# Kernel optimization log

Measured on AMD Instinct MI355X. Metric: run time of the kernel, lower is better.

The kernel has to match this reference:

```python
import jax, jax.numpy as jnp
import numpy as np

N_NODES = 50000
N_EDGES = 800000
F_IN = 32
H = 128
N_REL = 4
MAX_DEG = 10
N_GRAPHS = 64
N_BLOCKS = 2


def setup_inputs() -> dict:
    key = jax.random.key(0)
    ks = jax.random.split(key, 20)
    s = 0.05
    return {
        "x": jax.random.normal(ks[0], (N_NODES, F_IN), jnp.float32),
        "edge_index": jax.random.randint(ks[1], (2, N_EDGES), 0, N_NODES, dtype=jnp.int32),
        "edge_attr": jax.random.randint(ks[2], (N_EDGES,), 0, N_REL, dtype=jnp.int32),
        "batch_idx": jnp.sort(jax.random.randint(ks[3], (N_NODES,), 0, N_GRAPHS, dtype=jnp.int32)),
        "embed_W": jax.random.normal(ks[4], (F_IN, H), jnp.float32) * s,
        "embed_b": jax.random.normal(ks[5], (H,), jnp.float32) * s,
        "rgcn_Wrel": jax.random.normal(ks[6], (N_BLOCKS, N_REL, H, H), jnp.float32) * s,
        "rgcn_Wroot": jax.random.normal(ks[7], (N_BLOCKS, H, H), jnp.float32) * s,
        "rgcn_b": jax.random.normal(ks[8], (N_BLOCKS, H), jnp.float32) * s,
        "mf_Wl": jax.random.normal(ks[9], (N_BLOCKS, MAX_DEG + 1, H, H), jnp.float32) * s,
        "mf_bl": jax.random.normal(ks[10], (N_BLOCKS, MAX_DEG + 1, H), jnp.float32) * s,
        "mf_Wr": jax.random.normal(ks[11], (N_BLOCKS, MAX_DEG + 1, H, H), jnp.float32) * s,
        "lin1_W": jax.random.normal(ks[12], (H, H), jnp.float32) * s,
        "lin1_b": jax.random.normal(ks[13], (H,), jnp.float32) * s,
        "lin2_W": jax.random.normal(ks[14], (H, 1), jnp.float32) * s,
        "lin2_b": jax.random.normal(ks[15], (1,), jnp.float32) * s,
    }


def _rgcn(x, src, dst, rel, Wrel, Wroot, b):
    # PyG RGCNConv with default aggr='mean': per-relation mean over incoming
    # edges, then per-relation weight, plus root transform and bias.
    seg = dst * N_REL + rel  # composite segment id: (node, relation)
    agg = jax.ops.segment_sum(x[src], seg, num_segments=N_NODES * N_REL)
    cnt = jax.ops.segment_sum(jnp.ones((seg.shape[0],), x.dtype), seg,
                              num_segments=N_NODES * N_REL)
    agg = (agg / jnp.maximum(cnt, 1.0)[:, None]).reshape(N_NODES, N_REL, H)
    return jnp.einsum('nrh,rho->no', agg, Wrel) + x @ Wroot + b


def _mfconv(x, src, dst, Wl, bl, Wr):
    # PyG MFConv: sum-aggregate neighbors, then per-degree-bucket linear heads
    # (degree = in-degree clamped to MAX_DEG); lin_r applied to root x (no bias).
    h = jax.ops.segment_sum(x[src], dst, num_segments=N_NODES)  # [N,H]
    deg = jax.ops.segment_sum(jnp.ones((src.shape[0],), jnp.int32), dst,
                              num_segments=N_NODES)
    deg = jnp.minimum(deg, MAX_DEG)  # [N]
    # out_all: [D+1, N, H] candidate outputs, one per degree bucket
    out_all = (jnp.einsum('nh,dho->dno', h, Wl)
               + jnp.einsum('nh,dho->dno', x, Wr)
               + bl[:, None, :])
    return jnp.take_along_axis(out_all, deg[None, :, None], axis=0)[0]


def reference(x, edge_index, edge_attr, batch_idx, embed_W, embed_b,
              rgcn_Wrel, rgcn_Wroot, rgcn_b, mf_Wl, mf_bl, mf_Wr,
              lin1_W, lin1_b, lin2_W, lin2_b):
    src, dst = edge_index[0], edge_index[1]
    h = x @ embed_W + embed_b
    for blk in range(N_BLOCKS):
        if blk > 0:  # first block uses Identity instead of ReLU
            h = jax.nn.relu(h)
        h = _rgcn(h, src, dst, edge_attr, rgcn_Wrel[blk], rgcn_Wroot[blk], rgcn_b[blk])
        h = jax.nn.relu(h)
        h = _mfconv(h, src, dst, mf_Wl[blk], mf_bl[blk], mf_Wr[blk])
    g = jax.ops.segment_sum(h, batch_idx, num_segments=N_GRAPHS)  # global_add_pool
    g = jax.nn.relu(g @ lin1_W + lin1_b)
    return g @ lin2_W + lin2_b
```

## Files before the change

kernel.cpp:

```cpp
#include <hip/hip_runtime.h>
#include <hip/hip_bf16.h>

#define NRELS 4
#define MAXDEG 10
#define NBUCK 11
#define POOL_CHUNKS 8

typedef __attribute__((ext_vector_type(8))) short s16x8;
typedef __attribute__((ext_vector_type(4))) float f32x4;
typedef __attribute__((ext_vector_type(8))) unsigned short u16x8;

__device__ inline unsigned short f2b(float f) {
  __hip_bfloat16 h = __float2bfloat16(f);
  return *reinterpret_cast<unsigned short*>(&h);
}
__device__ inline float b2f(unsigned short u) {
  union { unsigned int i; float f; } v;
  v.i = ((unsigned int)u) << 16;
  return v.f;
}
__device__ inline float blo(unsigned int v) {
  union { unsigned int i; float f; } x;
  x.i = v << 16;
  return x.f;
}
__device__ inline float bhi(unsigned int v) {
  union { unsigned int i; float f; } x;
  x.i = v & 0xffff0000u;
  return x.f;
}

typedef __attribute__((address_space(3))) unsigned int lds_uint;
typedef __attribute__((address_space(1))) const unsigned int glob_uint;
__device__ __forceinline__ void gld_lds16(const void* g, void* l) {
  __builtin_amdgcn_global_load_lds((glob_uint*)g, (lds_uint*)l, 16, 0, 0);
}

__global__ __launch_bounds__(512) void coarse_count_scan(
    const int* __restrict__ dst, int* __restrict__ bhist, int* __restrict__ boff,
    int* __restrict__ bcur, int* __restrict__ done, int* __restrict__ perm, int permCap,
    int NB, int E, int nblocks) {
  __shared__ int lh[512];
  __shared__ int lastf;
  int t = threadIdx.x;
  lh[t] = 0;
  __syncthreads();
  for (int i = blockIdx.x * 512 + t; i < permCap; i += nblocks * 512) perm[i] = -1;
  int base = blockIdx.x * 4096;
  int lim = E - base;
  if (lim > 4096) lim = 4096;
  for (int i = t; i < lim; i += 512) atomicAdd(&lh[dst[base + i] >> 7], 1);
  __syncthreads();
  if (lh[t]) atomicAdd(&bhist[t], lh[t]);
  __threadfence();
  __syncthreads();
  if (t == 0) lastf = (atomicAdd(done, 1) == nblocks - 1) ? 1 : 0;
  __syncthreads();
  if (!lastf) return;
  int v = (t < NB) ? atomicAdd(&bhist[t], 0) : 0;
  lh[t] = v;
  __syncthreads();
  for (int o = 1; o < 512; o <<= 1) {
    int x = (t >= o) ? lh[t - o] : 0;
    __syncthreads();
    lh[t] += x;
    __syncthreads();
  }
  if (t < NB) {
    int st = lh[t] - v;
    boff[t] = st;
    bcur[t] = st;
  }
  if (t == 0) boff[NB] = E;
}

__global__ __launch_bounds__(512) void coarse_scatter(
    const int* __restrict__ src, const int* __restrict__ dst, const int* __restrict__ rel,
    int* __restrict__ bcur, uint2* __restrict__ ebuf, int E) {
  __shared__ int lhist[512];
  __shared__ int lstart[512];
  __shared__ int lcur[512];
  __shared__ int gbase[512];
  __shared__ uint2 stage[4096];
  int t = threadIdx.x;
  lhist[t] = 0;
  __syncthreads();
  int base = blockIdx.x * 4096;
  int lim = E - base;
  if (lim > 4096) lim = 4096;
  for (int i = t; i < lim; i += 512) atomicAdd(&lhist[dst[base + i] >> 7], 1);
  __syncthreads();
  int myc = lhist[t];
  lstart[t] = myc;
  __syncthreads();
  for (int o = 1; o < 512; o <<= 1) {
    int x = (t >= o) ? lstart[t - o] : 0;
    __syncthreads();
    lstart[t] += x;
    __syncthreads();
  }
  int incl = lstart[t];
  __syncthreads();
  lstart[t] = incl - myc;
  lcur[t] = 0;
  if (myc > 0) gbase[t] = atomicAdd(&bcur[t], myc);
  __syncthreads();
  for (int i = t; i < lim; i += 512) {
    int e = base + i;
    int d = dst[e];
    int b = d >> 7;
    int slot = lstart[b] + atomicAdd(&lcur[b], 1);
    stage[slot] = make_uint2((unsigned)(d * 4 + rel[e]), (unsigned)src[e]);
  }
  __syncthreads();
  for (int i = t; i < lim; i += 512) {
    uint2 val = stage[i];
    int b = (int)(val.x >> 9);
    ebuf[gbase[b] + (i - lstart[b])] = val;
  }
}

__global__ __launch_bounds__(512) void fine_place(
    const uint2* __restrict__ ebuf, const int* __restrict__ boff, int* __restrict__ cnt,
    int* __restrict__ seg_start, float* __restrict__ inv, int* __restrict__ deg,
    int* __restrict__ bucket, int* __restrict__ hist, int* __restrict__ csr, int NSEG) {
  __shared__ int lh[512];
  __shared__ int sc[512];
  __shared__ int lcur[512];
  __shared__ int lbh[16];
  int t = threadIdx.x;
  int b = blockIdx.x;
  lh[t] = 0;
  if (t < 16) lbh[t] = 0;
  __syncthreads();
  int s = boff[b], e = boff[b + 1];
  for (int i = s + t; i < e; i += 512) atomicAdd(&lh[ebuf[i].x & 511], 1);
  __syncthreads();
  int v = lh[t];
  sc[t] = v;
  __syncthreads();
  for (int o = 1; o < 512; o <<= 1) {
    int x = (t >= o) ? sc[t - o] : 0;
    __syncthreads();
    sc[t] += x;
    __syncthreads();
  }
  int gseg = b * 512 + t;
  int mystart = s + sc[t] - v;
  lcur[t] = mystart;
  if (gseg < NSEG) {
    cnt[gseg] = v;
    seg_start[gseg] = mystart;
    inv[gseg] = 1.0f / (float)(v > 1 ? v : 1);
    if ((t & 3) == 0) {
      int d = sc[t + 3] - sc[t] + v;
      int n = gseg >> 2;
      deg[n] = d;
      int bk = d < MAXDEG ? d : MAXDEG;
      bucket[n] = bk;
      atomicAdd(&lbh[bk], 1);
    }
  }
  __syncthreads();
  if (t < NBUCK && lbh[t]) atomicAdd(&hist[t], lbh[t]);
  for (int i = s + t; i < e; i += 512) {
    uint2 vv = ebuf[i];
    int pos = atomicAdd(&lcur[vv.x & 511], 1);
    csr[pos] = (int)vv.y;
  }
}

__global__ void build_perm(const int* __restrict__ bucket, const int* __restrict__ hist,
                           int* __restrict__ fill, int* __restrict__ perm, int N) {
  __shared__ int soff[NBUCK];
  if (threadIdx.x == 0) {
    int acc = 0;
    for (int b = 0; b < NBUCK; b++) {
      soff[b] = acc;
      acc += ((hist[b] + 63) >> 6) << 6;
    }
  }
  __syncthreads();
  int n = blockIdx.x * 256 + threadIdx.x;
  int b = (n < N) ? bucket[n] : -1;
  int lane = threadIdx.x & 63;
  for (int bb = 0; bb < NBUCK; bb++) {
    unsigned long long m = __ballot(b == bb);
    if (m == 0ULL) continue;
    int leader = __ffsll(m) - 1;
    int base = 0;
    if (lane == leader) base = atomicAdd(&fill[bb], __popcll(m));
    base = __shfl(base, leader);
    if (b == bb) {
      int idx = __popcll(m & ((1ULL << lane) - 1ULL));
      perm[soff[bb] + base + idx] = n;
    }
  }
}

__global__ __launch_bounds__(256) void embed_conv(
    const float* __restrict__ x, const float* __restrict__ embW,
    const float* __restrict__ bias, const float* __restrict__ Wrel,
    const float* __restrict__ Wroot, const float* __restrict__ Wl,
    const float* __restrict__ Wr, unsigned short* __restrict__ Bt,
    unsigned short* __restrict__ Btm, unsigned short* __restrict__ out, int N, int nbE) {
  if ((int)blockIdx.x >= nbE) {
    const int R1 = 2 * 128 * 640;
    const int R2 = R1 + 2 * 11 * 128 * 256;
    int t = (blockIdx.x - nbE) * 256 + threadIdx.x;
    if (t < R1) {
      int blk = t / 81920;
      int rem = t % 81920;
      int n = rem / 640;
      int k = rem % 640;
      float v;
      if (k < 512)
        v = Wrel[(size_t)blk * 65536 + (size_t)k * 128 + n];
      else
        v = Wroot[(size_t)blk * 16384 + (size_t)(k - 512) * 128 + n];
      Bt[t] = f2b(v);
    } else if (t < R2) {
      int t2 = t - R1;
      int k = t2 & 255;
      int n = (t2 >> 8) & 127;
      int bb = (t2 >> 15) % 11;
      int blk = t2 / (11 * 128 * 256);
      float v;
      if (k < 128)
        v = Wl[(((size_t)blk * 11 + bb) * 128 + k) * 128 + n];
      else
        v = Wr[(((size_t)blk * 11 + bb) * 128 + (k - 128)) * 128 + n];
      Btm[t2] = f2b(v);
    }
    return;
  }
  __shared__ unsigned char As[64 * 80];
  __shared__ unsigned char Bs[128 * 80];
  int t = threadIdx.x;
  int m0 = blockIdx.x * 64;
  {
    int r = t >> 2, s = t & 3;
    int gr = m0 + r;
    if (gr >= N) gr = N - 1;
    const float* xp = x + (size_t)gr * 32 + s * 8;
    float4 f0 = *(const float4*)xp;
    float4 f1 = *(const float4*)(xp + 4);
    u16x8 o;
    o[0] = f2b(f0.x); o[1] = f2b(f0.y); o[2] = f2b(f0.z); o[3] = f2b(f0.w);
    o[4] = f2b(f1.x); o[5] = f2b(f1.y); o[6] = f2b(f1.z); o[7] = f2b(f1.w);
    *(u16x8*)(As + r * 80 + s * 16) = o;
  }
  {
    int n = t >> 1, hf = t & 1;
    unsigned short tmp[16];
#pragma unroll
    for (int j = 0; j < 16; j++) tmp[j] = f2b(embW[(size_t)(hf * 16 + j) * 128 + n]);
    *(u16x8*)(Bs + n * 80 + hf * 32) = *(u16x8*)tmp;
    *(u16x8*)(Bs + n * 80 + hf * 32 + 16) = *(u16x8*)(tmp + 8);
  }
  __syncthreads();
  int lane = t & 63, wave = t >> 6;
  int row = lane & 15, quad = lane >> 4;
  int nh = wave * 32;
  f32x4 acc[2][4];
#pragma unroll
  for (int i = 0; i < 2; i++)
#pragma unroll
    for (int j = 0; j < 4; j++) acc[i][j] = (f32x4){0.f, 0.f, 0.f, 0.f};
  s16x8 af[4], bf[2];
#pragma unroll
  for (int mt = 0; mt < 4; mt++) {
    int R = mt * 16 + row;
    af[mt] = *(const s16x8*)(As + R * 80 + quad * 16);
  }
#pragma unroll
  for (int nt = 0; nt < 2; nt++) {
    int R = nh + nt * 16 + row;
    bf[nt] = *(const s16x8*)(Bs + R * 80 + quad * 16);
  }
#pragma unroll
  for (int nt = 0; nt < 2; nt++)
#pragma unroll
    for (int mt = 0; mt < 4; mt++)
      acc[nt][mt] = __builtin_amdgcn_mfma_f32_16x16x32_bf16(af[mt], bf[nt], acc[nt][mt], 0, 0, 0);
#pragma unroll
  for (int nt = 0; nt < 2; nt++) {
    int n = nh + nt * 16 + row;
    float bv = bias[n];
#pragma unroll
    for (int mt = 0; mt < 4; mt++) {
#pragma unroll
      for (int r4 = 0; r4 < 4; r4++) {
        int m = m0 + mt * 16 + quad * 4 + r4;
        if (m < N) out[(size_t)m * 128 + n] = f2b(acc[nt][mt][r4] + bv);
      }
    }
  }
}

#define ACC8(v)                                   \
  do {                                            \
    a0 += blo((v).x); a1 += bhi((v).x);           \
    a2 += blo((v).y); a3 += bhi((v).y);           \
    a4 += blo((v).z); a5 += bhi((v).z);           \
    a6 += blo((v).w); a7 += bhi((v).w);           \
  } while (0)

__global__ __launch_bounds__(256) void rgcn_gather(
    const unsigned short* __restrict__ hb, const int* __restrict__ csr,
    const int* __restrict__ seg_start, const int* __restrict__ cnt,
    const float* __restrict__ inv, const int* __restrict__ perm,
    unsigned short* __restrict__ ahat, int total) {
  int half = blockIdx.x & 1;
  int i = (blockIdx.x >> 1) * 32 + (threadIdx.x >> 3);
  if (i >= total) return;
  int n = perm[i];
  if (n < 0) return;
  int c8 = half * 64 + (threadIdx.x & 7) * 8;
  int4 st4 = *(const int4*)(seg_start + (size_t)n * 4);
  int4 cn4 = *(const int4*)(cnt + (size_t)n * 4);
  float4 w4 = *(const float4*)(inv + (size_t)n * 4);
  int sts[4] = {st4.x, st4.y, st4.z, st4.w};
  int cns[4] = {cn4.x, cn4.y, cn4.z, cn4.w};
  float ws[4] = {w4.x, w4.y, w4.z, w4.w};
#pragma unroll
  for (int r = 0; r < 4; r++) {
    int st = sts[r], cn = cns[r];
    float w = ws[r];
    float a0 = 0.f, a1 = 0.f, a2 = 0.f, a3 = 0.f, a4 = 0.f, a5 = 0.f, a6 = 0.f, a7 = 0.f;
    int ii = 0;
    for (; ii + 4 <= cn; ii += 4) {
      int p0 = csr[st + ii], p1 = csr[st + ii + 1];
      int p2 = csr[st + ii + 2], p3 = csr[st + ii + 3];
      uint4 v0 = *(const uint4*)(hb + (size_t)p0 * 128 + c8);
      uint4 v1 = *(const uint4*)(hb + (size_t)p1 * 128 + c8);
      uint4 v2 = *(const uint4*)(hb + (size_t)p2 * 128 + c8);
      uint4 v3 = *(const uint4*)(hb + (size_t)p3 * 128 + c8);
      ACC8(v0);
      ACC8(v1);
      ACC8(v2);
      ACC8(v3);
    }
    if (ii + 2 <= cn) {
      int p0 = csr[st + ii], p1 = csr[st + ii + 1];
      uint4 v0 = *(const uint4*)(hb + (size_t)p0 * 128 + c8);
      uint4 v1 = *(const uint4*)(hb + (size_t)p1 * 128 + c8);
      ACC8(v0);
      ACC8(v1);
      ii += 2;
    }
    if (ii < cn) {
      uint4 v0 = *(const uint4*)(hb + (size_t)csr[st + ii] * 128 + c8);
      ACC8(v0);
    }
    uint4 o;
    o.x = (unsigned int)f2b(a0 * w) | ((unsigned int)f2b(a1 * w) << 16);
    o.y = (unsigned int)f2b(a2 * w) | ((unsigned int)f2b(a3 * w) << 16);
    o.z = (unsigned int)f2b(a4 * w) | ((unsigned int)f2b(a5 * w) << 16);
    o.w = (unsigned int)f2b(a6 * w) | ((unsigned int)f2b(a7 * w) << 16);
    *(uint4*)(ahat + (size_t)i * 512 + r * 128 + c8) = o;
  }
}

__global__ __launch_bounds__(256) void mf_gather(
    const unsigned short* __restrict__ hb, const int* __restrict__ csr,
    const int* __restrict__ seg_start, const int* __restrict__ deg,
    const int* __restrict__ perm, unsigned short* __restrict__ amf, int total) {
  int half = blockIdx.x & 1;
  int i = (blockIdx.x >> 1) * 32 + (threadIdx.x >> 3);
  if (i >= total) return;
  int n = perm[i];
  if (n < 0) return;
  int c8 = half * 64 + (threadIdx.x & 7) * 8;
  int st = seg_start[n * 4], dg = deg[n];
  float a0 = 0.f, a1 = 0.f, a2 = 0.f, a3 = 0.f, a4 = 0.f, a5 = 0.f, a6 = 0.f, a7 = 0.f;
  int i2 = 0;
  for (; i2 + 4 <= dg; i2 += 4) {
    int p0 = csr[st + i2], p1 = csr[st + i2 + 1];
    int p2 = csr[st + i2 + 2], p3 = csr[st + i2 + 3];
    uint4 v0 = *(const uint4*)(hb + (size_t)p0 * 128 + c8);
    uint4 v1 = *(const uint4*)(hb + (size_t)p1 * 128 + c8);
    uint4 v2 = *(const uint4*)(hb + (size_t)p2 * 128 + c8);
    uint4 v3 = *(const uint4*)(hb + (size_t)p3 * 128 + c8);
    ACC8(v0);
    ACC8(v1);
    ACC8(v2);
    ACC8(v3);
  }
  if (i2 + 2 <= dg) {
    int p0 = csr[st + i2], p1 = csr[st + i2 + 1];
    uint4 v0 = *(const uint4*)(hb + (size_t)p0 * 128 + c8);
    uint4 v1 = *(const uint4*)(hb + (size_t)p1 * 128 + c8);
    ACC8(v0);
    ACC8(v1);
    i2 += 2;
  }
  if (i2 < dg) {
    uint4 v0 = *(const uint4*)(hb + (size_t)csr[st + i2] * 128 + c8);
    ACC8(v0);
  }
  uint4 o;
  o.x = (unsigned int)f2b(a0) | ((unsigned int)f2b(a1) << 16);
  o.y = (unsigned int)f2b(a2) | ((unsigned int)f2b(a3) << 16);
  o.z = (unsigned int)f2b(a4) | ((unsigned int)f2b(a5) << 16);
  o.w = (unsigned int)f2b(a6) | ((unsigned int)f2b(a7) << 16);
  *(uint4*)(amf + (size_t)i * 128 + c8) = o;
}

__global__ __launch_bounds__(256) void rgcn_mfma(const unsigned short* __restrict__ A,
                                                 const unsigned short* __restrict__ hroot,
                                                 const unsigned short* __restrict__ Bt,
                                                 const float* __restrict__ bias,
                                                 const int* __restrict__ perm,
                                                 unsigned short* __restrict__ out) {
  __shared__ unsigned char As[8192];
  __shared__ unsigned char Bs[16384];
  __shared__ int nodes[64];
  int t = threadIdx.x;
  int m0 = blockIdx.x * 64;
  if (t >= 64 && t < 128) nodes[t - 64] = perm[m0 + t - 64];
  __syncthreads();
  int lane = t & 63, wave = t >> 6;
  int row = lane & 15, quad = lane >> 4;
  int nh = wave * 32;
  f32x4 acc[2][4];
#pragma unroll
  for (int i = 0; i < 2; i++)
#pragma unroll
    for (int j = 0; j < 4; j++) acc[i][j] = (f32x4){0.f, 0.f, 0.f, 0.f};

  for (int kt = 0; kt < 10; kt++) {
    int kb2 = kt * 128;
#pragma unroll
    for (int s = 0; s < 2; s++) {
      int o = s * 4096 + t * 16;
      int r = o >> 7, c = ((o >> 4) & 7) ^ (r & 7);
      const char* gsrc;
      if (kt < 8) {
        gsrc = (const char*)A + (size_t)(m0 + r) * 1024 + kb2 + c * 16;
      } else {
        int nd = nodes[r];
        if (nd < 0) nd = 0;
        gsrc = (const char*)hroot + (size_t)nd * 256 + (kb2 - 1024) + c * 16;
      }
      gld_lds16(gsrc, As + o);
    }
#pragma unroll
    for (int s = 0; s < 4; s++) {
      int o = s * 4096 + t * 16;
      int r = o >> 7, c = ((o >> 4) & 7) ^ (r & 7);
      gld_lds16((const char*)Bt + (size_t)r * 1280 + kb2 + c * 16, Bs + o);
    }
    __syncthreads();
#pragma unroll
    for (int ks = 0; ks < 2; ks++) {
      int cch = ks * 4 + quad;
      s16x8 af[4], bf[2];
#pragma unroll
      for (int mt = 0; mt < 4; mt++) {
        int R = mt * 16 + row;
        af[mt] = *(const s16x8*)(As + R * 128 + ((cch ^ (R & 7)) << 4));
      }
#pragma unroll
      for (int nt = 0; nt < 2; nt++) {
        int R = nh + nt * 16 + row;
        bf[nt] = *(const s16x8*)(Bs + R * 128 + ((cch ^ (R & 7)) << 4));
      }
#pragma unroll
      for (int nt = 0; nt < 2; nt++)
#pragma unroll
        for (int mt = 0; mt < 4; mt++)
          acc[nt][mt] = __builtin_amdgcn_mfma_f32_16x16x32_bf16(af[mt], bf[nt], acc[nt][mt], 0, 0, 0);
    }
    __syncthreads();
  }
#pragma unroll
  for (int nt = 0; nt < 2; nt++) {
    int n = nh + nt * 16 + row;
    float bv = bias[n];
#pragma unroll
    for (int mt = 0; mt < 4; mt++) {
#pragma unroll
      for (int r4 = 0; r4 < 4; r4++) {
        int nd = nodes[mt * 16 + quad * 4 + r4];
        if (nd >= 0) out[(size_t)nd * 128 + n] = f2b(fmaxf(acc[nt][mt][r4] + bv, 0.f));
      }
    }
  }
}

__global__ __launch_bounds__(256) void mf_mfma(const unsigned short* __restrict__ A,
                                               const unsigned short* __restrict__ hroot,
                                               const unsigned short* __restrict__ Bt,
                                               const float* __restrict__ bl,
                                               const int* __restrict__ perm,
                                               const int* __restrict__ hist,
                                               unsigned short* __restrict__ out, int relu_out) {
  __shared__ unsigned char As[8192];
  __shared__ unsigned char Bs[16384];
  __shared__ int soff[NBUCK + 1];
  __shared__ int nodes[64];
  int t = threadIdx.x;
  int m0 = blockIdx.x * 64;
  if (t == 0) {
    int acc = 0;
    for (int b2 = 0; b2 < NBUCK; b2++) {
      soff[b2] = acc;
      acc += ((hist[b2] + 63) >> 6) << 6;
    }
    soff[NBUCK] = acc;
  }
  if (t >= 64 && t < 128) nodes[t - 64] = perm[m0 + t - 64];
  __syncthreads();
  if (m0 >= soff[NBUCK]) return;
  int b = 0;
  while (b < 10 && m0 >= soff[b + 1]) b++;
  const unsigned short* Bb = Bt + (size_t)b * 128 * 256;
  const float* bb = bl + b * 128;
  int lane = t & 63, wave = t >> 6;
  int row = lane & 15, quad = lane >> 4;
  int nh = wave * 32;
  f32x4 acc[2][4];
#pragma unroll
  for (int i = 0; i < 2; i++)
#pragma unroll
    for (int j = 0; j < 4; j++) acc[i][j] = (f32x4){0.f, 0.f, 0.f, 0.f};

  for (int kt = 0; kt < 4; kt++) {
    int kb2 = kt * 128;
#pragma unroll
    for (int s = 0; s < 2; s++) {
      int o = s * 4096 + t * 16;
      int r = o >> 7, c = ((o >> 4) & 7) ^ (r & 7);
      const char* gsrc;
      if (kt < 2) {
        gsrc = (const char*)A + (size_t)(m0 + r) * 256 + kb2 + c * 16;
      } else {
        int nd = nodes[r];
        if (nd < 0) nd = 0;
        gsrc = (const char*)hroot + (size_t)nd * 256 + (kb2 - 512) + c * 16;
      }
      gld_lds16(gsrc, As + o);
    }
#pragma unroll
    for (int s = 0; s < 4; s++) {
      int o = s * 4096 + t * 16;
      int r = o >> 7, c = ((o >> 4) & 7) ^ (r & 7);
      gld_lds16((const char*)Bb + (size_t)r * 512 + kb2 + c * 16, Bs + o);
    }
    __syncthreads();
#pragma unroll
    for (int ks = 0; ks < 2; ks++) {
      int cch = ks * 4 + quad;
      s16x8 af[4], bf[2];
#pragma unroll
      for (int mt = 0; mt < 4; mt++) {
        int R = mt * 16 + row;
        af[mt] = *(const s16x8*)(As + R * 128 + ((cch ^ (R & 7)) << 4));
      }
#pragma unroll
      for (int nt = 0; nt < 2; nt++) {
        int R = nh + nt * 16 + row;
        bf[nt] = *(const s16x8*)(Bs + R * 128 + ((cch ^ (R & 7)) << 4));
      }
#pragma unroll
      for (int nt = 0; nt < 2; nt++)
#pragma unroll
        for (int mt = 0; mt < 4; mt++)
          acc[nt][mt] = __builtin_amdgcn_mfma_f32_16x16x32_bf16(af[mt], bf[nt], acc[nt][mt], 0, 0, 0);
    }
    __syncthreads();
  }
#pragma unroll
  for (int nt = 0; nt < 2; nt++) {
    int n = nh + nt * 16 + row;
    float bv = bb[n];
#pragma unroll
    for (int mt = 0; mt < 4; mt++) {
#pragma unroll
      for (int r4 = 0; r4 < 4; r4++) {
        int nd = nodes[mt * 16 + quad * 4 + r4];
        if (nd >= 0) {
          float v = acc[nt][mt][r4] + bv;
          if (relu_out) v = fmaxf(v, 0.f);
          out[(size_t)nd * 128 + n] = f2b(v);
        }
      }
    }
  }
}

__global__ void pool2(const unsigned short* __restrict__ h, const int* __restrict__ batch,
                      float* __restrict__ g, int N, int G) {
  int gr = blockIdx.x / POOL_CHUNKS;
  int ck = blockIdx.x % POOL_CHUNKS;
  int t = threadIdx.x;
  int lane = t & 63, grp = t >> 6;
  int lo = 0, hi = N;
  while (lo < hi) {
    int m = (lo + hi) >> 1;
    if (batch[m] < gr) lo = m + 1; else hi = m;
  }
  int s = lo;
  lo = s; hi = N;
  while (lo < hi) {
    int m = (lo + hi) >> 1;
    if (batch[m] < gr + 1) lo = m + 1; else hi = m;
  }
  int e = lo;
  int len = e - s;
  int a = s + (int)(((long long)len * ck) / POOL_CHUNKS);
  int b = s + (int)(((long long)len * (ck + 1)) / POOL_CHUNKS);
  float s0 = 0.f, s1 = 0.f;
  for (int n = a + grp; n < b; n += 2) {
    unsigned int v = *(const unsigned int*)(h + (size_t)n * 128 + lane * 2);
    s0 += blo(v);
    s1 += bhi(v);
  }
  if (b > a + grp) {
    atomicAdd(&g[gr * 128 + lane * 2], s0);
    atomicAdd(&g[gr * 128 + lane * 2 + 1], s1);
  }
}

__global__ void head_kernel(const float* __restrict__ g, const float* __restrict__ W1,
                            const float* __restrict__ b1, const float* __restrict__ W2,
                            const float* __restrict__ b2, float* __restrict__ out) {
  int bg = blockIdx.x;
  int o = threadIdx.x;
  __shared__ float gs[128];
  __shared__ float red[128];
  gs[o] = g[bg * 128 + o];
  __syncthreads();
  float acc = b1[o];
  for (int k = 0; k < 128; k++) acc += gs[k] * W1[k * 128 + o];
  acc = fmaxf(acc, 0.f);
  red[o] = acc * W2[o];
  __syncthreads();
  for (int s = 64; s > 0; s >>= 1) {
    if (o < s) red[o] += red[o + s];
    __syncthreads();
  }
  if (o == 0) out[bg] = red[0] + b2[0];
}

extern "C" void kernel_launch(void* const* d_in, const int* in_sizes, int n_in,
                              void* d_out, int out_size, void* d_ws, size_t ws_size,
                              hipStream_t stream) {
  const float* x = (const float*)d_in[0];
  const int* ei = (const int*)d_in[1];
  const int* ea = (const int*)d_in[2];
  const int* batch = (const int*)d_in[3];
  const float* embW = (const float*)d_in[4];
  const float* embB = (const float*)d_in[5];
  const float* Wrel = (const float*)d_in[6];
  const float* Wroot = (const float*)d_in[7];
  const float* rb = (const float*)d_in[8];
  const float* Wl = (const float*)d_in[9];
  const float* bl = (const float*)d_in[10];
  const float* Wr = (const float*)d_in[11];
  const float* l1W = (const float*)d_in[12];
  const float* l1b = (const float*)d_in[13];
  const float* l2W = (const float*)d_in[14];
  const float* l2b = (const float*)d_in[15];
  float* out = (float*)d_out;

  int N = in_sizes[0] / 32;
  int E = in_sizes[2];
  int G = out_size;
  int NSEG = N * 4;
  int NB = (N + 127) >> 7;

  char* p = (char*)d_ws;
  auto alloc = [&](size_t bytes) {
    char* r = p;
    p += (bytes + 255) & ~(size_t)255;
    return r;
  };
  int permCap = ((N + 63) / 64 + NBUCK) * 64;
  unsigned short* h_bf = (unsigned short*)alloc((size_t)N * 128 * 2);
  unsigned short* h2_bf = (unsigned short*)alloc((size_t)N * 128 * 2);
  unsigned short* ahat = (unsigned short*)alloc((size_t)permCap * 512 * 2);
  unsigned short* amf = (unsigned short*)alloc((size_t)permCap * 128 * 2);
  unsigned short* Btr = (unsigned short*)alloc((size_t)2 * 128 * 640 * 2);
  unsigned short* Btm = (unsigned short*)alloc((size_t)2 * 11 * 128 * 256 * 2);
  float* inv = (float*)alloc((size_t)NSEG * 4);
  int* cnt = (int*)alloc((size_t)NSEG * 4);
  int* seg_start = (int*)alloc((size_t)NSEG * 4);
  int* csr = (int*)alloc((size_t)E * 4);
  uint2* ebuf = (uint2*)alloc((size_t)E * 8);
  int* deg = (int*)alloc((size_t)N * 4);
  int* bucket = (int*)alloc((size_t)N * 4);
  int* perm = (int*)alloc((size_t)permCap * 4);
  int* boff = (int*)alloc(516 * 4);
  int* bcur = (int*)alloc(512 * 4);
  size_t zeroBytes = 8192 + (size_t)G * 128 * 4;
  char* zb = alloc(zeroBytes);
  int* bhist = (int*)zb;
  int* hist = (int*)(zb + 4096);
  int* fill = (int*)(zb + 4224);
  int* done = (int*)(zb + 4352);
  float* g = (float*)(zb + 8192);

  (void)hipMemsetAsync(zb, 0, zeroBytes, stream);

  const int* src = ei;
  const int* dst = ei + E;

  int sblocks = (E + 4095) / 4096;
  coarse_count_scan<<<sblocks, 512, 0, stream>>>(dst, bhist, boff, bcur, done, perm, permCap,
                                                 NB, E, sblocks);
  coarse_scatter<<<sblocks, 512, 0, stream>>>(src, dst, ea, bcur, ebuf, E);
  fine_place<<<NB, 512, 0, stream>>>(ebuf, boff, cnt, seg_start, inv, deg, bucket, hist, csr,
                                     NSEG);
  build_perm<<<(N + 255) / 256, 256, 0, stream>>>(bucket, hist, fill, perm, N);

  int nbE = (N + 63) / 64;
  int convBlocks = (2 * 128 * 640 + 2 * 11 * 128 * 256 + 255) / 256;
  embed_conv<<<nbE + convBlocks, 256, 0, stream>>>(x, embW, embB, Wrel, Wroot, Wl, Wr, Btr,
                                                   Btm, h_bf, N, nbE);

  int mfblocks = permCap / 64;
  int gblocks = ((permCap + 31) / 32) * 2;
  for (int blk = 0; blk < 2; blk++) {
    rgcn_gather<<<gblocks, 256, 0, stream>>>(h_bf, csr, seg_start, cnt, inv, perm, ahat,
                                             permCap);
    rgcn_mfma<<<mfblocks, 256, 0, stream>>>(ahat, h_bf, Btr + (size_t)blk * 81920,
                                            rb + blk * 128, perm, h2_bf);
    mf_gather<<<gblocks, 256, 0, stream>>>(h2_bf, csr, seg_start, deg, perm, amf, permCap);
    mf_mfma<<<mfblocks, 256, 0, stream>>>(amf, h2_bf, Btm + (size_t)blk * 11 * 128 * 256,
                                          bl + (size_t)blk * 11 * 128, perm, hist, h_bf,
                                          (blk == 0) ? 1 : 0);
  }
  pool2<<<G * POOL_CHUNKS, 128, 0, stream>>>(h_bf, batch, g, N, G);
  head_kernel<<<G, 128, 0, stream>>>(g, l1W, l1b, l2W, l2b, out);
}
```

Baseline: 396.7 us.

## Fuse neighbor gathers into MFMA GEMM kernels, dropping intermediate aggregate buffers

The separate gather kernels for RGCN and MFConv aggregation are merged into their MFMA GEMM kernels. Each block now gathers its 64 nodes' neighbor sums straight into a swizzled LDS A-tile, one relation at a time, before running the matrix multiply. This removes the global write and re-read of the ahat and amf intermediates and two launches per block. In exchange, each thread gathers 16 channels, so memory-level parallelism is lower, the gather is serialized with the MFMA work under barriers, and the kernel uses more LDS.

```diff
diff --git a/kernel.cpp b/kernel.cpp
--- a/kernel.cpp
+++ b/kernel.cpp
@@ -298,182 +298,148 @@
   }
 }
 
-#define ACC8(v)                                   \
-  do {                                            \
-    a0 += blo((v).x); a1 += bhi((v).x);           \
-    a2 += blo((v).y); a3 += bhi((v).y);           \
-    a4 += blo((v).z); a5 += bhi((v).z);           \
-    a6 += blo((v).w); a7 += bhi((v).w);           \
-  } while (0)
-
-__global__ __launch_bounds__(256) void rgcn_gather(
+__device__ __forceinline__ void acc8v(float* a, uint4 v) {
+  a[0] += blo(v.x); a[1] += bhi(v.x);
+  a[2] += blo(v.y); a[3] += bhi(v.y);
+  a[4] += blo(v.z); a[5] += bhi(v.z);
+  a[6] += blo(v.w); a[7] += bhi(v.w);
+}
+
+__device__ __forceinline__ void gather_seg(const unsigned short* __restrict__ hb,
+                                           const int* __restrict__ csr, int st, int cn,
+                                           int chunk, float* a) {
+  const unsigned short* hq = hb + chunk * 16;
+  int i = 0;
+  for (; i + 2 <= cn; i += 2) {
+    int p0 = csr[st + i], p1 = csr[st + i + 1];
+    const uint4* r0 = (const uint4*)(hq + (size_t)p0 * 128);
+    const uint4* r1 = (const uint4*)(hq + (size_t)p1 * 128);
+    uint4 v00 = r0[0], v01 = r0[1];
+    uint4 v10 = r1[0], v11 = r1[1];
+    acc8v(a + 0, v00); acc8v(a + 8, v01);
+    acc8v(a + 0, v10); acc8v(a + 8, v11);
+  }
+  if (i < cn) {
+    const uint4* r0 = (const uint4*)(hq + (size_t)csr[st + i] * 128);
+    acc8v(a + 0, r0[0]); acc8v(a + 8, r0[1]);
+  }
+}
+
+__device__ __forceinline__ void write_frag(unsigned char* Ag, int ln, int chunk,
+                                           const float* a, float w) {
+  int s = chunk >> 2;
+#pragma unroll
+  for (int h = 0; h < 2; h++) {
+    int c = (((chunk & 3) * 2 + h)) ^ (ln & 7);
+    const float* p = a + h * 8;
+    uint4 o;
+    o.x = (unsigned int)f2b(p[0] * w) | ((unsigned int)f2b(p[1] * w) << 16);
+    o.y = (unsigned int)f2b(p[2] * w) | ((unsigned int)f2b(p[3] * w) << 16);
+    o.z = (unsigned int)f2b(p[4] * w) | ((unsigned int)f2b(p[5] * w) << 16);
+    o.w = (unsigned int)f2b(p[6] * w) | ((unsigned int)f2b(p[7] * w) << 16);
+    *(uint4*)(Ag + s * 8192 + ln * 128 + (c << 4)) = o;
+  }
+}
+
+__device__ __forceinline__ void gemm_tile(const unsigned char* Areg, const unsigned char* Breg,
+                                          int row, int quad, int nh, f32x4 acc[2][4]) {
+#pragma unroll
+  for (int s = 0; s < 2; s++) {
+#pragma unroll
+    for (int ks = 0; ks < 2; ks++) {
+      int cch = ks * 4 + quad;
+      s16x8 af[4], bf[2];
+#pragma unroll
+      for (int mt = 0; mt < 4; mt++) {
+        int R = mt * 16 + row;
+        af[mt] = *(const s16x8*)(Areg + s * 8192 + R * 128 + ((cch ^ (R & 7)) << 4));
+      }
+#pragma unroll
+      for (int nt = 0; nt < 2; nt++) {
+        int R = nh + nt * 16 + row;
+        bf[nt] = *(const s16x8*)(Breg + s * 16384 + R * 128 + ((cch ^ (R & 7)) << 4));
+      }
+#pragma unroll
+      for (int nt = 0; nt < 2; nt++)
+#pragma unroll
+        for (int mt = 0; mt < 4; mt++)
+          acc[nt][mt] = __builtin_amdgcn_mfma_f32_16x16x32_bf16(af[mt], bf[nt], acc[nt][mt], 0, 0, 0);
+    }
+  }
+}
+
+__global__ __launch_bounds__(256) void rgcn_fused(
     const unsigned short* __restrict__ hb, const int* __restrict__ csr,
     const int* __restrict__ seg_start, const int* __restrict__ cnt,
     const float* __restrict__ inv, const int* __restrict__ perm,
-    unsigned short* __restrict__ ahat, int total) {
-  int half = blockIdx.x & 1;
-  int i = (blockIdx.x >> 1) * 32 + (threadIdx.x >> 3);
-  if (i >= total) return;
-  int n = perm[i];
-  if (n < 0) return;
-  int c8 = half * 64 + (threadIdx.x & 7) * 8;
-  int4 st4 = *(const int4*)(seg_start + (size_t)n * 4);
-  int4 cn4 = *(const int4*)(cnt + (size_t)n * 4);
-  float4 w4 = *(const float4*)(inv + (size_t)n * 4);
-  int sts[4] = {st4.x, st4.y, st4.z, st4.w};
-  int cns[4] = {cn4.x, cn4.y, cn4.z, cn4.w};
-  float ws[4] = {w4.x, w4.y, w4.z, w4.w};
-#pragma unroll
-  for (int r = 0; r < 4; r++) {
-    int st = sts[r], cn = cns[r];
-    float w = ws[r];
-    float a0 = 0.f, a1 = 0.f, a2 = 0.f, a3 = 0.f, a4 = 0.f, a5 = 0.f, a6 = 0.f, a7 = 0.f;
-    int ii = 0;
-    for (; ii + 4 <= cn; ii += 4) {
-      int p0 = csr[st + ii], p1 = csr[st + ii + 1];
-      int p2 = csr[st + ii + 2], p3 = csr[st + ii + 3];
-      uint4 v0 = *(const uint4*)(hb + (size_t)p0 * 128 + c8);
-      uint4 v1 = *(const uint4*)(hb + (size_t)p1 * 128 + c8);
-      uint4 v2 = *(const uint4*)(hb + (size_t)p2 * 128 + c8);
-      uint4 v3 = *(const uint4*)(hb + (size_t)p3 * 128 + c8);
-      ACC8(v0);
-      ACC8(v1);
-      ACC8(v2);
-      ACC8(v3);
-    }
-    if (ii + 2 <= cn) {
-      int p0 = csr[st + ii], p1 = csr[st + ii + 1];
-      uint4 v0 = *(const uint4*)(hb + (size_t)p0 * 128 + c8);
-      uint4 v1 = *(const uint4*)(hb + (size_t)p1 * 128 + c8);
-      ACC8(v0);
-      ACC8(v1);
-      ii += 2;
-    }
-    if (ii < cn) {
-      uint4 v0 = *(const uint4*)(hb + (size_t)csr[st + ii] * 128 + c8);
-      ACC8(v0);
-    }
-    uint4 o;
-    o.x = (unsigned int)f2b(a0 * w) | ((unsigned int)f2b(a1 * w) << 16);
-    o.y = (unsigned int)f2b(a2 * w) | ((unsigned int)f2b(a3 * w) << 16);
-    o.z = (unsigned int)f2b(a4 * w) | ((unsigned int)f2b(a5 * w) << 16);
-    o.w = (unsigned int)f2b(a6 * w) | ((unsigned int)f2b(a7 * w) << 16);
-    *(uint4*)(ahat + (size_t)i * 512 + r * 128 + c8) = o;
-  }
-}
-
-__global__ __launch_bounds__(256) void mf_gather(
-    const unsigned short* __restrict__ hb, const int* __restrict__ csr,
-    const int* __restrict__ seg_start, const int* __restrict__ deg,
-    const int* __restrict__ perm, unsigned short* __restrict__ amf, int total) {
-  int half = blockIdx.x & 1;
-  int i = (blockIdx.x >> 1) * 32 + (threadIdx.x >> 3);
-  if (i >= total) return;
-  int n = perm[i];
-  if (n < 0) return;
-  int c8 = half * 64 + (threadIdx.x & 7) * 8;
-  int st = seg_start[n * 4], dg = deg[n];
-  float a0 = 0.f, a1 = 0.f, a2 = 0.f, a3 = 0.f, a4 = 0.f, a5 = 0.f, a6 = 0.f, a7 = 0.f;
-  int i2 = 0;
-  for (; i2 + 4 <= dg; i2 += 4) {
-    int p0 = csr[st + i2], p1 = csr[st + i2 + 1];
-    int p2 = csr[st + i2 + 2], p3 = csr[st + i2 + 3];
-    uint4 v0 = *(const uint4*)(hb + (size_t)p0 * 128 + c8);
-    uint4 v1 = *(const uint4*)(hb + (size_t)p1 * 128 + c8);
-    uint4 v2 = *(const uint4*)(hb + (size_t)p2 * 128 + c8);
-    uint4 v3 = *(const uint4*)(hb + (size_t)p3 * 128 + c8);
-    ACC8(v0);
-    ACC8(v1);
-    ACC8(v2);
-    ACC8(v3);
-  }
-  if (i2 + 2 <= dg) {
-    int p0 = csr[st + i2], p1 = csr[st + i2 + 1];
-    uint4 v0 = *(const uint4*)(hb + (size_t)p0 * 128 + c8);
-    uint4 v1 = *(const uint4*)(hb + (size_t)p1 * 128 + c8);
-    ACC8(v0);
-    ACC8(v1);
-    i2 += 2;
-  }
-  if (i2 < dg) {
-    uint4 v0 = *(const uint4*)(hb + (size_t)csr[st + i2] * 128 + c8);
-    ACC8(v0);
-  }
-  uint4 o;
-  o.x = (unsigned int)f2b(a0) | ((unsigned int)f2b(a1) << 16);
-  o.y = (unsigned int)f2b(a2) | ((unsigned int)f2b(a3) << 16);
-  o.z = (unsigned int)f2b(a4) | ((unsigned int)f2b(a5) << 16);
-  o.w = (unsigned int)f2b(a6) | ((unsigned int)f2b(a7) << 16);
-  *(uint4*)(amf + (size_t)i * 128 + c8) = o;
-}
-
-__global__ __launch_bounds__(256) void rgcn_mfma(const unsigned short* __restrict__ A,
-                                                 const unsigned short* __restrict__ hroot,
-                                                 const unsigned short* __restrict__ Bt,
-                                                 const float* __restrict__ bias,
-                                                 const int* __restrict__ perm,
-                                                 unsigned short* __restrict__ out) {
-  __shared__ unsigned char As[8192];
-  __shared__ unsigned char Bs[16384];
+    const unsigned short* __restrict__ Bt, const float* __restrict__ bias,
+    unsigned short* __restrict__ out) {
+  __shared__ unsigned char Ag[16384];
+  __shared__ unsigned char Bs[32768];
   __shared__ int nodes[64];
   int t = threadIdx.x;
   int m0 = blockIdx.x * 64;
-  if (t >= 64 && t < 128) nodes[t - 64] = perm[m0 + t - 64];
+  if (t < 64) nodes[t] = perm[m0 + t];
   __syncthreads();
   int lane = t & 63, wave = t >> 6;
   int row = lane & 15, quad = lane >> 4;
   int nh = wave * 32;
+  int chunk = t & 7, lnb = t >> 3;
   f32x4 acc[2][4];
 #pragma unroll
   for (int i = 0; i < 2; i++)
 #pragma unroll
     for (int j = 0; j < 4; j++) acc[i][j] = (f32x4){0.f, 0.f, 0.f, 0.f};
 
-  for (int kt = 0; kt < 10; kt++) {
-    int kb2 = kt * 128;
-#pragma unroll
-    for (int s = 0; s < 2; s++) {
-      int o = s * 4096 + t * 16;
-      int r = o >> 7, c = ((o >> 4) & 7) ^ (r & 7);
-      const char* gsrc;
-      if (kt < 8) {
-        gsrc = (const char*)A + (size_t)(m0 + r) * 1024 + kb2 + c * 16;
-      } else {
-        int nd = nodes[r];
-        if (nd < 0) nd = 0;
-        gsrc = (const char*)hroot + (size_t)nd * 256 + (kb2 - 1024) + c * 16;
+  for (int rel = 0; rel < 4; rel++) {
+#pragma unroll
+    for (int s = 0; s < 2; s++)
+#pragma unroll
+      for (int p = 0; p < 4; p++) {
+        int o = s * 16384 + p * 4096 + t * 16;
+        int r = (o >> 7) & 127, c = ((o >> 4) & 7) ^ (r & 7);
+        gld_lds16((const char*)Bt + (size_t)r * 1280 + rel * 256 + s * 128 + c * 16, Bs + o);
       }
-      gld_lds16(gsrc, As + o);
-    }
-#pragma unroll
-    for (int s = 0; s < 4; s++) {
-      int o = s * 4096 + t * 16;
-      int r = o >> 7, c = ((o >> 4) & 7) ^ (r & 7);
-      gld_lds16((const char*)Bt + (size_t)r * 1280 + kb2 + c * 16, Bs + o);
-    }
-    __syncthreads();
-#pragma unroll
-    for (int ks = 0; ks < 2; ks++) {
-      int cch = ks * 4 + quad;
-      s16x8 af[4], bf[2];
-#pragma unroll
-      for (int mt = 0; mt < 4; mt++) {
-        int R = mt * 16 + row;
-        af[mt] = *(const s16x8*)(As + R * 128 + ((cch ^ (R & 7)) << 4));
+#pragma unroll
+    for (int pp = 0; pp < 2; pp++) {
+      int ln = pp * 32 + lnb;
+      int nd = nodes[ln];
+      float a[16];
+#pragma unroll
+      for (int j = 0; j < 16; j++) a[j] = 0.f;
+      float w = 1.f;
+      if (nd >= 0) {
+        int sid = nd * 4 + rel;
+        int st = seg_start[sid], cn2 = cnt[sid];
+        w = inv[sid];
+        gather_seg(hb, csr, st, cn2, chunk, a);
       }
-#pragma unroll
-      for (int nt = 0; nt < 2; nt++) {
-        int R = nh + nt * 16 + row;
-        bf[nt] = *(const s16x8*)(Bs + R * 128 + ((cch ^ (R & 7)) << 4));
-      }
-#pragma unroll
-      for (int nt = 0; nt < 2; nt++)
-#pragma unroll
-        for (int mt = 0; mt < 4; mt++)
-          acc[nt][mt] = __builtin_amdgcn_mfma_f32_16x16x32_bf16(af[mt], bf[nt], acc[nt][mt], 0, 0, 0);
-    }
-    __syncthreads();
-  }
+      write_frag(Ag, ln, chunk, a, w);
+    }
+    __syncthreads();
+    gemm_tile(Ag, Bs, row, quad, nh, acc);
+    __syncthreads();
+  }
+#pragma unroll
+  for (int s = 0; s < 2; s++)
+#pragma unroll
+    for (int p = 0; p < 4; p++) {
+      int o = s * 16384 + p * 4096 + t * 16;
+      int r = (o >> 7) & 127, c = ((o >> 4) & 7) ^ (r & 7);
+      gld_lds16((const char*)Bt + (size_t)r * 1280 + 1024 + s * 128 + c * 16, Bs + o);
+    }
+#pragma unroll
+  for (int s = 0; s < 2; s++)
+#pragma unroll
+    for (int p = 0; p < 2; p++) {
+      int o = s * 8192 + p * 4096 + t * 16;
+      int r = (o >> 7) & 63, c = ((o >> 4) & 7) ^ (r & 7);
+      int nd = nodes[r];
+      if (nd < 0) nd = 0;
+      gld_lds16((const char*)hb + (size_t)nd * 256 + s * 128 + c * 16, Ag + o);
+    }
+  __syncthreads();
+  gemm_tile(Ag, Bs, row, quad, nh, acc);
 #pragma unroll
   for (int nt = 0; nt < 2; nt++) {
     int n = nh + nt * 16 + row;
@@ -489,88 +455,83 @@
   }
 }
 
-__global__ __launch_bounds__(256) void mf_mfma(const unsigned short* __restrict__ A,
-                                               const unsigned short* __restrict__ hroot,
-                                               const unsigned short* __restrict__ Bt,
-                                               const float* __restrict__ bl,
-                                               const int* __restrict__ perm,
-                                               const int* __restrict__ hist,
-                                               unsigned short* __restrict__ out, int relu_out) {
-  __shared__ unsigned char As[8192];
-  __shared__ unsigned char Bs[16384];
+__global__ __launch_bounds__(256) void mf_fused(
+    const unsigned short* __restrict__ hb, const int* __restrict__ csr,
+    const int* __restrict__ seg_start, const int* __restrict__ deg,
+    const int* __restrict__ perm, const int* __restrict__ hist,
+    const unsigned short* __restrict__ Bt, const float* __restrict__ bl,
+    unsigned short* __restrict__ out, int relu_out) {
+  __shared__ unsigned char Ag[16384];
+  __shared__ unsigned char Bs[32768];
+  __shared__ int nodes[64];
   __shared__ int soff[NBUCK + 1];
-  __shared__ int nodes[64];
   int t = threadIdx.x;
   int m0 = blockIdx.x * 64;
   if (t == 0) {
-    int acc = 0;
+    int a2 = 0;
     for (int b2 = 0; b2 < NBUCK; b2++) {
-      soff[b2] = acc;
-      acc += ((hist[b2] + 63) >> 6) << 6;
-    }
-    soff[NBUCK] = acc;
-  }
-  if (t >= 64 && t < 128) nodes[t - 64] = perm[m0 + t - 64];
+      soff[b2] = a2;
+      a2 += ((hist[b2] + 63) >> 6) << 6;
+    }
+    soff[NBUCK] = a2;
+  }
+  if (t < 64) nodes[t] = perm[m0 + t];
   __syncthreads();
   if (m0 >= soff[NBUCK]) return;
   int b = 0;
   while (b < 10 && m0 >= soff[b + 1]) b++;
   const unsigned short* Bb = Bt + (size_t)b * 128 * 256;
-  const float* bb = bl + b * 128;
+#pragma unroll
+  for (int s = 0; s < 2; s++)
+#pragma unroll
+    for (int p = 0; p < 4; p++) {
+      int o = s * 16384 + p * 4096 + t * 16;
+      int r = (o >> 7) & 127, c = ((o >> 4) & 7) ^ (r & 7);
+      gld_lds16((const char*)Bb + (size_t)r * 512 + s * 128 + c * 16, Bs + o);
+    }
   int lane = t & 63, wave = t >> 6;
   int row = lane & 15, quad = lane >> 4;
   int nh = wave * 32;
+  int chunk = t & 7, lnb = t >> 3;
   f32x4 acc[2][4];
 #pragma unroll
   for (int i = 0; i < 2; i++)
 #pragma unroll
     for (int j = 0; j < 4; j++) acc[i][j] = (f32x4){0.f, 0.f, 0.f, 0.f};
-
-  for (int kt = 0; kt < 4; kt++) {
-    int kb2 = kt * 128;
-#pragma unroll
-    for (int s = 0; s < 2; s++) {
-      int o = s * 4096 + t * 16;
-      int r = o >> 7, c = ((o >> 4) & 7) ^ (r & 7);
-      const char* gsrc;
-      if (kt < 2) {
-        gsrc = (const char*)A + (size_t)(m0 + r) * 256 + kb2 + c * 16;
-      } else {
-        int nd = nodes[r];
-        if (nd < 0) nd = 0;
-        gsrc = (const char*)hroot + (size_t)nd * 256 + (kb2 - 512) + c * 16;
-      }
-      gld_lds16(gsrc, As + o);
-    }
-#pragma unroll
-    for (int s = 0; s < 4; s++) {
-      int o = s * 4096 + t * 16;
-      int r = o >> 7, c = ((o >> 4) & 7) ^ (r & 7);
-      gld_lds16((const char*)Bb + (size_t)r * 512 + kb2 + c * 16, Bs + o);
-    }
-    __syncthreads();
-#pragma unroll
-    for (int ks = 0; ks < 2; ks++) {
-      int cch = ks * 4 + quad;
-      s16x8 af[4], bf[2];
-#pragma unroll
-      for (int mt = 0; mt < 4; mt++) {
-        int R = mt * 16 + row;
-        af[mt] = *(const s16x8*)(As + R * 128 + ((cch ^ (R & 7)) << 4));
-      }
-#pragma unroll
-      for (int nt = 0; nt < 2; nt++) {
-        int R = nh + nt * 16 + row;
-        bf[nt] = *(const s16x8*)(Bs + R * 128 + ((cch ^ (R & 7)) << 4));
-      }
-#pragma unroll
-      for (int nt = 0; nt < 2; nt++)
-#pragma unroll
-        for (int mt = 0; mt < 4; mt++)
-          acc[nt][mt] = __builtin_amdgcn_mfma_f32_16x16x32_bf16(af[mt], bf[nt], acc[nt][mt], 0, 0, 0);
-    }
-    __syncthreads();
-  }
+#pragma unroll
+  for (int pp = 0; pp < 2; pp++) {
+    int ln = pp * 32 + lnb;
+    int nd = nodes[ln];
+    float a[16];
+#pragma unroll
+    for (int j = 0; j < 16; j++) a[j] = 0.f;
+    if (nd >= 0) gather_seg(hb, csr, seg_start[nd * 4], deg[nd], chunk, a);
+    write_frag(Ag, ln, chunk, a, 1.f);
+  }
+  __syncthreads();
+  gemm_tile(Ag, Bs, row, quad, nh, acc);
+  __syncthreads();
+#pragma unroll
+  for (int s = 0; s < 2; s++)
+#pragma unroll
+    for (int p = 0; p < 4; p++) {
+      int o = s * 16384 + p * 4096 + t * 16;
+      int r = (o >> 7) & 127, c = ((o >> 4) & 7) ^ (r & 7);
+      gld_lds16((const char*)Bb + (size_t)r * 512 + 256 + s * 128 + c * 16, Bs + o);
+    }
+#pragma unroll
+  for (int s = 0; s < 2; s++)
+#pragma unroll
+    for (int p = 0; p < 2; p++) {
+      int o = s * 8192 + p * 4096 + t * 16;
+      int r = (o >> 7) & 63, c = ((o >> 4) & 7) ^ (r & 7);
+      int nd = nodes[r];
+      if (nd < 0) nd = 0;
+      gld_lds16((const char*)hb + (size_t)nd * 256 + s * 128 + c * 16, Ag + o);
+    }
+  __syncthreads();
+  gemm_tile(Ag, Bs, row, quad, nh, acc);
+  const float* bb = bl + b * 128;
 #pragma unroll
   for (int nt = 0; nt < 2; nt++) {
     int n = nh + nt * 16 + row;
@@ -680,8 +641,6 @@
   int permCap = ((N + 63) / 64 + NBUCK) * 64;
   unsigned short* h_bf = (unsigned short*)alloc((size_t)N * 128 * 2);
   unsigned short* h2_bf = (unsigned short*)alloc((size_t)N * 128 * 2);
-  unsigned short* ahat = (unsigned short*)alloc((size_t)permCap * 512 * 2);
-  unsigned short* amf = (unsigned short*)alloc((size_t)permCap * 128 * 2);
   unsigned short* Btr = (unsigned short*)alloc((size_t)2 * 128 * 640 * 2);
   unsigned short* Btm = (unsigned short*)alloc((size_t)2 * 11 * 128 * 256 * 2);
   float* inv = (float*)alloc((size_t)NSEG * 4);
@@ -721,16 +680,14 @@
                                                    Btm, h_bf, N, nbE);
 
   int mfblocks = permCap / 64;
-  int gblocks = ((permCap + 31) / 32) * 2;
   for (int blk = 0; blk < 2; blk++) {
-    rgcn_gather<<<gblocks, 256, 0, stream>>>(h_bf, csr, seg_start, cnt, inv, perm, ahat,
-                                             permCap);
-    rgcn_mfma<<<mfblocks, 256, 0, stream>>>(ahat, h_bf, Btr + (size_t)blk * 81920,
-                                            rb + blk * 128, perm, h2_bf);
-    mf_gather<<<gblocks, 256, 0, stream>>>(h2_bf, csr, seg_start, deg, perm, amf, permCap);
-    mf_mfma<<<mfblocks, 256, 0, stream>>>(amf, h2_bf, Btm + (size_t)blk * 11 * 128 * 256,
-                                          bl + (size_t)blk * 11 * 128, perm, hist, h_bf,
-                                          (blk == 0) ? 1 : 0);
+    rgcn_fused<<<mfblocks, 256, 0, stream>>>(h_bf, csr, seg_start, cnt, inv, perm,
+                                             Btr + (size_t)blk * 81920, rb + blk * 128,
+                                             h2_bf);
+    mf_fused<<<mfblocks, 256, 0, stream>>>(h2_bf, csr, seg_start, deg, perm, hist,
+                                           Btm + (size_t)blk * 11 * 128 * 256,
+                                           bl + (size_t)blk * 11 * 128, h_bf,
+                                           (blk == 0) ? 1 : 0);
   }
   pool2<<<G * POOL_CHUNKS, 128, 0, stream>>>(h_bf, batch, g, N, G);
   head_kernel<<<G, 128, 0, stream>>>(g, l1W, l1b, l2W, l2b, out);
```

Result: slower. 472.4 us (+19.1%).
